# Optimization experiments

Hardware: AMD Instinct MI355X
Metric: run time of the kernel (lower is better)

The kernel has to match this reference:

```python
import jax, jax.numpy as jnp
import numpy as np

NUM_CAPS = 8
NITER = 3
TAU = 1.0
N_NODES = 50000
N_EDGES = 800000
D_FEAT = 128


def _l2norm(v):
    # matches torch fn.normalize(dim=-1, eps=1e-12): v / max(||v||, eps)
    n = jnp.linalg.norm(v, axis=-1, keepdims=True)
    return v / jnp.maximum(n, 1e-12)


def setup_inputs() -> dict:
    key = jax.random.key(0)
    k1, k2, k3 = jax.random.split(key, 3)
    x = jax.random.normal(k1, (N_NODES, D_FEAT), dtype=jnp.float32)
    src = jax.random.randint(k2, (N_EDGES,), 0, N_NODES)
    trg = jax.random.randint(k3, (N_EDGES,), 0, N_NODES)
    edge_index = jnp.stack([src, trg], axis=0).astype(jnp.int64)
    return {"x": x, "edge_index": edge_index}


def reference(x, edge_index):
    num_node, num_dim = x.shape
    dpc = num_dim // NUM_CAPS  # dim per capsule
    src, trg = edge_index[0], edge_index[1]

    xc = _l2norm(x.reshape(num_node, NUM_CAPS, dpc))  # [N, C, d]
    z = xc[src]                                        # [E, C, d] gathered source caps
    u = xc
    for _ in range(NITER):
        # per-edge, per-capsule agreement score
        p = jnp.einsum('ecd,ecd->ec', z, u[trg])       # [E, C]
        p = jax.nn.softmax(p / TAU, axis=1)
        msg = z * p[:, :, None]                        # [E, C, d]
        u = jax.ops.segment_sum(msg, trg, num_segments=num_node)  # [N, C, d]
        u = _l2norm(u + xc)
    return u.reshape(num_node, num_dim)
```

## Files before the change

kernel.cpp:

```cpp
#include <hip/hip_runtime.h>
#include <hip/hip_bf16.h>

#define DF   128
#define DPC  16
#define KCAP 62
#define RWRD 32

#define NB_ROUTE 1024
#define NB_PREP  2048
#define NB_ZERO  257

__device__ __forceinline__ float cap_sum(float v) {
    v += __shfl_xor(v, 1);
    v += __shfl_xor(v, 2);
    v += __shfl_xor(v, 4);
    return v;
}
__device__ __forceinline__ float bits_lo(unsigned int w) {
    union { unsigned int u; float f; } c; c.u = w << 16; return c.f;
}
__device__ __forceinline__ float bits_hi(unsigned int w) {
    union { unsigned int u; float f; } c; c.u = w & 0xFFFF0000u; return c.f;
}
__device__ __forceinline__ unsigned int f2b_pack(float lo, float hi) {
    __hip_bfloat16 a = __float2bfloat16(lo), b = __float2bfloat16(hi);
    unsigned short ua = *reinterpret_cast<unsigned short*>(&a);
    unsigned short ub = *reinterpret_cast<unsigned short*>(&b);
    return ((unsigned int)ub << 16) | ua;
}
__device__ __forceinline__ float2 load_x2(const void* __restrict__ xraw, int fp32,
                                          int node, int lane) {
    size_t off = (size_t)node * DF + (size_t)lane * 2;
    if (fp32) {
        return *reinterpret_cast<const float2*>((const float*)xraw + off);
    } else {
        unsigned int w = ((const unsigned int*)xraw)[(size_t)node * 64 + lane];
        return make_float2(bits_lo(w), bits_hi(w));
    }
}
__device__ __forceinline__ int2 edge_st(const int* __restrict__ ei, int i64,
                                        int e, int n_edges) {
    size_t si = i64 ? (size_t)2 * e             : (size_t)e;
    size_t ti = i64 ? (size_t)2 * (n_edges + e) : (size_t)(n_edges + e);
    return make_int2(ei[si], ei[ti]);
}
__device__ __forceinline__ void cvt16(const uint4& w0, const uint4& w1, float* z) {
    z[0]  = bits_lo(w0.x); z[1]  = bits_hi(w0.x);
    z[2]  = bits_lo(w0.y); z[3]  = bits_hi(w0.y);
    z[4]  = bits_lo(w0.z); z[5]  = bits_hi(w0.z);
    z[6]  = bits_lo(w0.w); z[7]  = bits_hi(w0.w);
    z[8]  = bits_lo(w1.x); z[9]  = bits_hi(w1.x);
    z[10] = bits_lo(w1.y); z[11] = bits_hi(w1.y);
    z[12] = bits_lo(w1.z); z[13] = bits_hi(w1.z);
    z[14] = bits_lo(w1.w); z[15] = bits_hi(w1.w);
}
__device__ __forceinline__ void proc_chunk(const uint4& w0, const uint4& w1,
                                           bool valid, const float* u, float* acc) {
    float z[DPC];
    cvt16(w0, w1, z);
    float p = 0.0f;
    #pragma unroll
    for (int j = 0; j < DPC; ++j) p = fmaf(z[j], u[j], p);
    float ex = __expf(p);
    float sd = ex;
    sd += __shfl_xor(sd, 1);
    sd += __shfl_xor(sd, 2);
    sd += __shfl_xor(sd, 4);
    float w = valid ? ex * __builtin_amdgcn_rcpf(sd) : 0.0f;
    #pragma unroll
    for (int j = 0; j < DPC; ++j) acc[j] = fmaf(w, z[j], acc[j]);
}

__global__ void k_detect_zero(const unsigned int* __restrict__ xw,
                              const unsigned int* __restrict__ ew,
                              int* __restrict__ flags, int* __restrict__ bkt,
                              int n_nodes) {
    if (blockIdx.x == 0) {
        __shared__ int s_nan, s_zero;
        int tid = threadIdx.x;
        if (tid == 0) { s_nan = 0; s_zero = 0; }
        __syncthreads();
        int cnt_nan = 0;
        for (int i = tid; i < 4096; i += 256) {
            unsigned int lo = xw[i] & 0xFFFFu;
            if ((lo & 0x7F80u) == 0x7F80u) cnt_nan++;
        }
        int cnt_zero = 0;
        for (int i = tid; i < 1024; i += 256) {
            if (ew[2 * i + 1] == 0u) cnt_zero++;
        }
        atomicAdd(&s_nan, cnt_nan);
        atomicAdd(&s_zero, cnt_zero);
        __syncthreads();
        if (tid == 0) {
            flags[0] = (s_nan > 0) ? 1 : 0;
            flags[1] = (s_zero > 512) ? 1 : 0;
        }
    } else {
        int total = n_nodes * (RWRD / 4);
        int stride = (NB_ZERO - 1) * 256;
        for (int i = (blockIdx.x - 1) * 256 + threadIdx.x; i < total; i += stride)
            reinterpret_cast<uint4*>(bkt)[i] = make_uint4(0u, 0u, 0u, 0u);
    }
}

__global__ void k_prep(const void* __restrict__ xraw, unsigned int* __restrict__ xcb,
                       const int* __restrict__ ei, int* __restrict__ bkt,
                       const int* __restrict__ flags,
                       int n_nodes, int n_edges) {
    const int fp32 = flags[0];
    const int lane = threadIdx.x & 63;
    const int gw   = (blockIdx.x * blockDim.x + threadIdx.x) >> 6;
    const int nw   = (gridDim.x * blockDim.x) >> 6;

    for (int wid = gw; wid < n_nodes; wid += nw) {
        float2 v = load_x2(xraw, fp32, wid, lane);
        float ss = cap_sum(v.x * v.x + v.y * v.y);
        float scale = 1.0f / fmaxf(sqrtf(ss), 1e-12f);
        int c = lane >> 3, jp = lane & 7;
        int w = (jp < 4) ? (c * 4 + jp) : (32 + c * 4 + (jp - 4));
        xcb[(size_t)wid * 64 + w] = f2b_pack(v.x * scale, v.y * scale);
    }

    const int i64 = flags[1];
    const int gtid = blockIdx.x * blockDim.x + threadIdx.x;
    const int gth  = gridDim.x * blockDim.x;
    for (int e = gtid; e < n_edges; e += gth) {
        int2 st = edge_st(ei, i64, e, n_edges);
        if ((unsigned)st.x < (unsigned)n_nodes &&
            (unsigned)st.y < (unsigned)n_nodes) {
            int slot = atomicAdd(&bkt[(size_t)st.y * RWRD], 1);
            if (slot < KCAP)
                ((unsigned short*)&bkt[(size_t)st.y * RWRD])[2 + slot] =
                    (unsigned short)st.x;
        }
    }
}

__global__ void __launch_bounds__(256)
__attribute__((amdgpu_waves_per_eu(4, 4)))
k_route(const int* __restrict__ bkt,
        const unsigned int* __restrict__ xcb,
        float* __restrict__ u_out, int n_nodes) {
    const int lane = threadIdx.x & 63;
    const int gw   = (blockIdx.x * blockDim.x + threadIdx.x) >> 6;
    const int nw   = (gridDim.x * blockDim.x) >> 6;
    const int e8 = lane >> 3;
    const int c  = lane & 7;
    const int coff = c * 16;
    const char* __restrict__ xb = (const char*)xcb;

    for (int t = gw; t < n_nodes; t += nw) {
        unsigned rw = ((const unsigned*)(bkt + (size_t)t * RWRD))[lane & 31];

        size_t trow = (size_t)t << 8;
        uint4 t0 = *reinterpret_cast<const uint4*>(xb + trow + coff);
        uint4 t1 = *reinterpret_cast<const uint4*>(xb + trow + 128 + coff);

        int deg = __builtin_amdgcn_readfirstlane((int)rw);
        deg = min(deg, KCAP);

        auto nid = [&](int s) -> int {
            int g = 4 + 2 * s;
            unsigned wv = __shfl(rw, (lane & 32) | (g >> 2));
            return (int)((g & 2) ? (wv >> 16) : (wv & 0xFFFFu));
        };
        auto ldc = [&](int k, uint4& a, uint4& b) {
            int s  = e8 + 8 * k;
            int sl = (s < deg) ? s : 0;
            int off = nid(sl) << 8;
            a = *reinterpret_cast<const uint4*>(xb + off + coff);
            b = *reinterpret_cast<const uint4*>(xb + off + 128 + coff);
        };

        uint4 k0a, k0b, k1a, k1b, k2a, k2b;
        if (deg > 0)  ldc(0, k0a, k0b);
        if (deg > 8)  ldc(1, k1a, k1b);
        if (deg > 16) ldc(2, k2a, k2b);

        float xt[DPC], u[DPC];
        cvt16(t0, t1, xt);
        float ss = 0.0f;
        #pragma unroll
        for (int j = 0; j < DPC; ++j) ss = fmaf(xt[j], xt[j], ss);
        float sc = __builtin_amdgcn_rsqf(fmaxf(ss, 1e-24f));
        #pragma unroll
        for (int j = 0; j < DPC; ++j) { xt[j] *= sc; u[j] = xt[j]; }

        for (int it = 0; it < 3; ++it) {
            float acc[DPC];
            #pragma unroll
            for (int j = 0; j < DPC; ++j) acc[j] = 0.0f;

            if (deg > 0)  proc_chunk(k0a, k0b, e8 < deg,      u, acc);
            if (deg > 8)  proc_chunk(k1a, k1b, 8  + e8 < deg, u, acc);
            if (deg > 16) proc_chunk(k2a, k2b, 16 + e8 < deg, u, acc);
            if (deg > 24) {
                for (int base = 24; base < deg; base += 8) {
                    uint4 a, b;
                    ldc(base >> 3, a, b);
                    proc_chunk(a, b, base + e8 < deg, u, acc);
                }
            }

            #pragma unroll
            for (int j = 0; j < DPC; ++j) {
                acc[j] += __shfl_xor(acc[j], 8);
                acc[j] += __shfl_xor(acc[j], 16);
                acc[j] += __shfl_xor(acc[j], 32);
            }
            float s2 = 0.0f;
            #pragma unroll
            for (int j = 0; j < DPC; ++j) {
                u[j] = acc[j] + xt[j];
                s2 = fmaf(u[j], u[j], s2);
            }
            float sc2 = __builtin_amdgcn_rsqf(fmaxf(s2, 1e-24f));
            #pragma unroll
            for (int j = 0; j < DPC; ++j) u[j] *= sc2;
        }

        if (e8 == 0) {
            float* dst = u_out + (size_t)t * DF + c * DPC;
            #pragma unroll
            for (int j = 0; j < DPC; j += 4)
                *reinterpret_cast<float4*>(dst + j) =
                    make_float4(u[j], u[j+1], u[j+2], u[j+3]);
        }
    }
}

extern "C" void kernel_launch(void* const* d_in, const int* in_sizes, int n_in,
                              void* d_out, int out_size, void* d_ws, size_t ws_size,
                              hipStream_t stream) {
    const void* x  = d_in[0];
    const int*  ei = (const int*)d_in[1];
    const int n_nodes = in_sizes[0] / DF;
    const int n_edges = in_sizes[1] / 2;
    const size_t NC = (size_t)n_nodes * DF;

    unsigned int* xcb = (unsigned int*)d_ws;
    int* bkt   = (int*)(xcb + NC / 2);
    int* flags = bkt + (size_t)n_nodes * RWRD;

    float* u_out = (float*)d_out;

    k_detect_zero<<<NB_ZERO, 256, 0, stream>>>(
        (const unsigned int*)x, (const unsigned int*)ei, flags, bkt, n_nodes);
    k_prep<<<NB_PREP, 256, 0, stream>>>(x, xcb, ei, bkt, flags,
                                        n_nodes, n_edges);
    k_route<<<NB_ROUTE, 256, 0, stream>>>(bkt, xcb, u_out, n_nodes);
}
```

Before: 279.4 us.

## Reload neighbor capsules per iteration to cut registers and raise occupancy

```diff
diff --git a/kernel.cpp b/kernel.cpp
--- a/kernel.cpp
+++ b/kernel.cpp
@@ -6,7 +6,7 @@
 #define KCAP 62
 #define RWRD 32
 
-#define NB_ROUTE 1024
+#define NB_ROUTE 2048
 #define NB_PREP  2048
 #define NB_ZERO  257
 
@@ -44,23 +44,15 @@
     size_t ti = i64 ? (size_t)2 * (n_edges + e) : (size_t)(n_edges + e);
     return make_int2(ei[si], ei[ti]);
 }
-__device__ __forceinline__ void cvt16(const uint4& w0, const uint4& w1, float* z) {
-    z[0]  = bits_lo(w0.x); z[1]  = bits_hi(w0.x);
-    z[2]  = bits_lo(w0.y); z[3]  = bits_hi(w0.y);
-    z[4]  = bits_lo(w0.z); z[5]  = bits_hi(w0.z);
-    z[6]  = bits_lo(w0.w); z[7]  = bits_hi(w0.w);
-    z[8]  = bits_lo(w1.x); z[9]  = bits_hi(w1.x);
-    z[10] = bits_lo(w1.y); z[11] = bits_hi(w1.y);
-    z[12] = bits_lo(w1.z); z[13] = bits_hi(w1.z);
-    z[14] = bits_lo(w1.w); z[15] = bits_hi(w1.w);
-}
-__device__ __forceinline__ void proc_chunk(const uint4& w0, const uint4& w1,
-                                           bool valid, const float* u, float* acc) {
-    float z[DPC];
-    cvt16(w0, w1, z);
+__device__ __forceinline__ void proc_pk(const uint4& w0, const uint4& w1,
+                                        bool valid, const float* u, float* acc) {
+    unsigned ww[8] = {w0.x, w0.y, w0.z, w0.w, w1.x, w1.y, w1.z, w1.w};
     float p = 0.0f;
     #pragma unroll
-    for (int j = 0; j < DPC; ++j) p = fmaf(z[j], u[j], p);
+    for (int q = 0; q < 8; ++q) {
+        p = fmaf(bits_lo(ww[q]), u[2*q],   p);
+        p = fmaf(bits_hi(ww[q]), u[2*q+1], p);
+    }
     float ex = __expf(p);
     float sd = ex;
     sd += __shfl_xor(sd, 1);
@@ -68,7 +60,10 @@
     sd += __shfl_xor(sd, 4);
     float w = valid ? ex * __builtin_amdgcn_rcpf(sd) : 0.0f;
     #pragma unroll
-    for (int j = 0; j < DPC; ++j) acc[j] = fmaf(w, z[j], acc[j]);
+    for (int q = 0; q < 8; ++q) {
+        acc[2*q]   = fmaf(w, bits_lo(ww[q]), acc[2*q]);
+        acc[2*q+1] = fmaf(w, bits_hi(ww[q]), acc[2*q+1]);
+    }
 }
 
 __global__ void k_detect_zero(const unsigned int* __restrict__ xw,
@@ -129,16 +124,18 @@
         int2 st = edge_st(ei, i64, e, n_edges);
         if ((unsigned)st.x < (unsigned)n_nodes &&
             (unsigned)st.y < (unsigned)n_nodes) {
-            int slot = atomicAdd(&bkt[(size_t)st.y * RWRD], 1);
-            if (slot < KCAP)
-                ((unsigned short*)&bkt[(size_t)st.y * RWRD])[2 + slot] =
-                    (unsigned short)st.x;
+            unsigned* row = (unsigned*)(bkt + (size_t)st.y * RWRD);
+            int slot = atomicAdd((int*)row, 1);
+            if (slot < KCAP) {
+                int us   = 2 + slot;
+                unsigned val = (unsigned)(unsigned short)st.x << (16 * (us & 1));
+                atomicOr(row + (us >> 1), val);
+            }
         }
     }
 }
 
 __global__ void __launch_bounds__(256)
-__attribute__((amdgpu_waves_per_eu(4, 4)))
 k_route(const int* __restrict__ bkt,
         const unsigned int* __restrict__ xcb,
         float* __restrict__ u_out, int n_nodes) {
@@ -165,41 +162,64 @@
             unsigned wv = __shfl(rw, (lane & 32) | (g >> 2));
             return (int)((g & 2) ? (wv >> 16) : (wv & 0xFFFFu));
         };
-        auto ldc = [&](int k, uint4& a, uint4& b) {
-            int s  = e8 + 8 * k;
-            int sl = (s < deg) ? s : 0;
-            int off = nid(sl) << 8;
-            a = *reinterpret_cast<const uint4*>(xb + off + coff);
-            b = *reinterpret_cast<const uint4*>(xb + off + 128 + coff);
-        };
-
-        uint4 k0a, k0b, k1a, k1b, k2a, k2b;
-        if (deg > 0)  ldc(0, k0a, k0b);
-        if (deg > 8)  ldc(1, k1a, k1b);
-        if (deg > 16) ldc(2, k2a, k2b);
-
-        float xt[DPC], u[DPC];
-        cvt16(t0, t1, xt);
+
+        int off0 = 0, off1 = 0, off2 = 0;
+        {
+            int s0 = e8,      c0 = (s0 < deg) ? s0 : 0;
+            int s1 = e8 + 8,  c1 = (s1 < deg) ? s1 : 0;
+            int s2 = e8 + 16, c2 = (s2 < deg) ? s2 : 0;
+            if (deg > 0)  off0 = nid(c0) << 8;
+            if (deg > 8)  off1 = nid(c1) << 8;
+            if (deg > 16) off2 = nid(c2) << 8;
+        }
+
+        unsigned tw[8] = {t0.x, t0.y, t0.z, t0.w, t1.x, t1.y, t1.z, t1.w};
         float ss = 0.0f;
         #pragma unroll
-        for (int j = 0; j < DPC; ++j) ss = fmaf(xt[j], xt[j], ss);
+        for (int q = 0; q < 8; ++q) {
+            float xl = bits_lo(tw[q]), xh = bits_hi(tw[q]);
+            ss = fmaf(xl, xl, ss);
+            ss = fmaf(xh, xh, ss);
+        }
         float sc = __builtin_amdgcn_rsqf(fmaxf(ss, 1e-24f));
+        float u[DPC];
         #pragma unroll
-        for (int j = 0; j < DPC; ++j) { xt[j] *= sc; u[j] = xt[j]; }
+        for (int q = 0; q < 8; ++q) {
+            u[2*q]   = bits_lo(tw[q]) * sc;
+            u[2*q+1] = bits_hi(tw[q]) * sc;
+        }
 
         for (int it = 0; it < 3; ++it) {
+            asm volatile("" ::: "memory");
+
+            uint4 a0, b0, a1, b1, a2, b2;
+            if (deg > 0) {
+                a0 = *reinterpret_cast<const uint4*>(xb + off0 + coff);
+                b0 = *reinterpret_cast<const uint4*>(xb + off0 + 128 + coff);
+            }
+            if (deg > 8) {
+                a1 = *reinterpret_cast<const uint4*>(xb + off1 + coff);
+                b1 = *reinterpret_cast<const uint4*>(xb + off1 + 128 + coff);
+            }
             float acc[DPC];
             #pragma unroll
             for (int j = 0; j < DPC; ++j) acc[j] = 0.0f;
 
-            if (deg > 0)  proc_chunk(k0a, k0b, e8 < deg,      u, acc);
-            if (deg > 8)  proc_chunk(k1a, k1b, 8  + e8 < deg, u, acc);
-            if (deg > 16) proc_chunk(k2a, k2b, 16 + e8 < deg, u, acc);
+            if (deg > 0)  proc_pk(a0, b0, e8 < deg, u, acc);
+            if (deg > 16) {
+                a2 = *reinterpret_cast<const uint4*>(xb + off2 + coff);
+                b2 = *reinterpret_cast<const uint4*>(xb + off2 + 128 + coff);
+            }
+            if (deg > 8)  proc_pk(a1, b1, 8  + e8 < deg, u, acc);
+            if (deg > 16) proc_pk(a2, b2, 16 + e8 < deg, u, acc);
             if (deg > 24) {
                 for (int base = 24; base < deg; base += 8) {
-                    uint4 a, b;
-                    ldc(base >> 3, a, b);
-                    proc_chunk(a, b, base + e8 < deg, u, acc);
+                    int s  = base + e8;
+                    int sl = (s < deg) ? s : 0;
+                    int off = nid(sl) << 8;
+                    uint4 a = *reinterpret_cast<const uint4*>(xb + off + coff);
+                    uint4 b = *reinterpret_cast<const uint4*>(xb + off + 128 + coff);
+                    proc_pk(a, b, s < deg, u, acc);
                 }
             }
 
@@ -211,9 +231,13 @@
             }
             float s2 = 0.0f;
             #pragma unroll
-            for (int j = 0; j < DPC; ++j) {
-                u[j] = acc[j] + xt[j];
-                s2 = fmaf(u[j], u[j], s2);
+            for (int q = 0; q < 8; ++q) {
+                float xl = bits_lo(tw[q]) * sc;
+                float xh = bits_hi(tw[q]) * sc;
+                u[2*q]   = acc[2*q]   + xl;
+                u[2*q+1] = acc[2*q+1] + xh;
+                s2 = fmaf(u[2*q],   u[2*q],   s2);
+                s2 = fmaf(u[2*q+1], u[2*q+1], s2);
             }
             float sc2 = __builtin_amdgcn_rsqf(fmaxf(s2, 1e-24f));
             #pragma unroll
```

Result: no change. 280.9 us (+0.5%).
